# Optimization experiments

Hardware: AMD Instinct MI355X
Metric: run time of the kernel (lower is better)

## Reference

```python
import jax, jax.numpy as jnp
import numpy as np

OBS, H, F1, A, T, B = 128, 128, 256, 18, 128, 1024


def _ln(x, w, b, eps=1e-5):
    mu = jnp.mean(x, -1, keepdims=True)
    xc = x - mu
    var = jnp.mean(xc * xc, -1, keepdims=True)
    return xc * jax.lax.rsqrt(var + eps) * w + b


def _features(x, w1, b1, w2, b2, lnw, lnb):
    h = jax.nn.relu(x @ w1.T + b1)      # [N, 256]
    h = h @ w2.T + b2                   # [N, 128]
    return jax.nn.relu(_ln(h, lnw, lnb))


def _masked_lstm(xs, ds, h0, c0, wih, whh, b):
    # xs: [T,B,H], ds: [T,B] float; PyTorch gate order i,f,g,o
    def step(carry, inp):
        h, c = carry
        xt, dt = inp
        m = (1.0 - dt)[:, None]
        h = h * m
        c = c * m
        g = xt @ wih.T + h @ whh.T + b  # [B, 4H]
        i, f, gg, o = jnp.split(g, 4, axis=-1)
        c = jax.nn.sigmoid(f) * c + jax.nn.sigmoid(i) * jnp.tanh(gg)
        h = jax.nn.sigmoid(o) * jnp.tanh(c)
        return (h, c), h
    (hT, cT), hs = jax.lax.scan(step, (h0, c0), (xs, ds))
    return hs, hT, cT


def setup_inputs() -> dict:
    key = jax.random.key(0)
    ks = iter(jax.random.split(key, 64))
    p = lambda shape, s=0.05: jax.random.normal(next(ks), shape, jnp.float32) * s
    inp = {
        'x': jax.random.normal(next(ks), (T * B, OBS), jnp.float32),
        'actor_h': jnp.zeros((1, B, H), jnp.float32),
        'actor_c': jnp.zeros((1, B, H), jnp.float32),
        'critic_h': jnp.zeros((1, B, H), jnp.float32),
        'critic_c': jnp.zeros((1, B, H), jnp.float32),
        'done': jax.random.randint(next(ks), (T * B,), 0, 2, jnp.int32),
        'action': jax.random.randint(next(ks), (T * B,), 0, A, jnp.int64),
        # actor params
        'af_w1': p((F1, OBS)), 'af_b1': p((F1,)),
        'af_w2': p((H, F1)), 'af_b2': p((H,)),
        'af_lnw': jnp.ones((H,), jnp.float32), 'af_lnb': jnp.zeros((H,), jnp.float32),
        'a_wih': p((4 * H, H)), 'a_whh': p((4 * H, H)), 'a_b': p((4 * H,)),
        'a_lnw': jnp.ones((H,), jnp.float32), 'a_lnb': jnp.zeros((H,), jnp.float32),
        'a_hw': p((A, H)), 'a_hb': p((A,)),
        # critic params
        'cf_w1': p((F1, OBS)), 'cf_b1': p((F1,)),
        'cf_w2': p((H, F1)), 'cf_b2': p((H,)),
        'cf_lnw': jnp.ones((H,), jnp.float32), 'cf_lnb': jnp.zeros((H,), jnp.float32),
        'c_wih': p((4 * H, H)), 'c_whh': p((4 * H, H)), 'c_b': p((4 * H,)),
        'c_lnw': jnp.ones((H,), jnp.float32), 'c_lnb': jnp.zeros((H,), jnp.float32),
        'c_hw': p((1, H)), 'c_hb': p((1,)),
    }
    return inp


def reference(x, actor_h, actor_c, critic_h, critic_c,
              af_w1, af_b1, af_w2, af_b2, af_lnw, af_lnb,
              a_wih, a_whh, a_b, a_lnw, a_lnb, a_hw, a_hb,
              cf_w1, cf_b1, cf_w2, cf_b2, cf_lnw, cf_lnb,
              c_wih, c_whh, c_b, c_lnw, c_lnb, c_hw, c_hb,
              done, action):
    bsz = actor_h.shape[1]
    ds = done.astype(jnp.float32).reshape(-1, bsz)  # [T, B]

    # actor branch
    af = _features(x, af_w1, af_b1, af_w2, af_b2, af_lnw, af_lnb).reshape(-1, bsz, H)
    hs, ahT, acT = _masked_lstm(af, ds, actor_h[0], actor_c[0], a_wih, a_whh, a_b)
    ah = _ln(hs.reshape(-1, H), a_lnw, a_lnb)
    logits = ah @ a_hw.T + a_hb                     # [N, A]
    logp_all = jax.nn.log_softmax(logits)
    logp = jnp.take_along_axis(logp_all, action[:, None], axis=1)[:, 0]
    entropy = -jnp.sum(jnp.exp(logp_all) * logp_all, axis=-1)

    # critic branch
    cf = _features(x, cf_w1, cf_b1, cf_w2, cf_b2, cf_lnw, cf_lnb).reshape(-1, bsz, H)
    cs, chT, ccT = _masked_lstm(cf, ds, critic_h[0], critic_c[0], c_wih, c_whh, c_b)
    ch = _ln(cs.reshape(-1, H), c_lnw, c_lnb)
    value = ch @ c_hw.T + c_hb                      # [N, 1]

    return (action, logp, entropy, value,
            ahT[None], acT[None], chT[None], ccT[None])
```

## Files before the change

### kernel.cpp

```cpp
#include <hip/hip_runtime.h>
#include <stdint.h>
#include <stddef.h>

#define OBS 128
#define F1D 256
#define HD  128
#define NA  18
#define TT  128
#define BB  1024
#define NN  (TT*BB)
#define LOG2E 1.442695041f

typedef __attribute__((ext_vector_type(8))) short short8;
typedef __attribute__((ext_vector_type(4))) float f32x4;

__device__ __forceinline__ unsigned short f2bf(float f) {
  union { float f; uint32_t u; } v; v.f = f;
  uint32_t u = v.u;
  u += 0x7fffu + ((u >> 16) & 1u);
  return (unsigned short)(u >> 16);
}
__device__ __forceinline__ float bf2f(uint32_t hu) {
  union { uint32_t u; float f; } v; v.u = hu << 16;
  return v.f;
}
__device__ __forceinline__ uint32_t pk2(float lo, float hi) {
  uint32_t r;
  asm("v_cvt_pk_bf16_f32 %0, %1, %2" : "=v"(r) : "v"(lo), "v"(hi));
  return r;
}
__device__ __forceinline__ f32x4 mfma16(short8 a, short8 b, f32x4 c) {
  return __builtin_amdgcn_mfma_f32_16x16x32_bf16(a, b, c, 0, 0, 0);
}
__device__ __forceinline__ short8 cvt8(const float* p, float sc) {
  float4 a = *(const float4*)p;
  float4 b = *(const float4*)(p + 4);
  union { uint32_t u[4]; short8 s; } o;
  o.u[0] = pk2(a.x*sc, a.y*sc);
  o.u[1] = pk2(a.z*sc, a.w*sc);
  o.u[2] = pk2(b.x*sc, b.y*sc);
  o.u[3] = pk2(b.z*sc, b.w*sc);
  return o.s;
}
__device__ __forceinline__ short8 pin(short8 v) {
  int4 i = *(int4*)&v;
  asm volatile("" : "+v"(i.x), "+v"(i.y), "+v"(i.z), "+v"(i.w));
  return *(short8*)&i;
}

__global__ __launch_bounds__(512, 2) void feat_kernel(
    const float* __restrict__ x,
    const float* __restrict__ aw1, const float* __restrict__ ab1,
    const float* __restrict__ aw2, const float* __restrict__ ab2,
    const float* __restrict__ aflnw, const float* __restrict__ aflnb,
    const float* __restrict__ cw1, const float* __restrict__ cb1,
    const float* __restrict__ cw2, const float* __restrict__ cb2,
    const float* __restrict__ cflnw, const float* __restrict__ cflnb,
    unsigned short* __restrict__ featg)
{
  int g = blockIdx.x;
  int br = g >> 7;
  int chunk = g & 127;
  int base8 = chunk * 8;

  const float* w1  = br ? cw1 : aw1;
  const float* b1  = br ? cb1 : ab1;
  const float* w2  = br ? cw2 : aw2;
  const float* b2  = br ? cb2 : ab2;
  const float* flw = br ? cflnw : aflnw;
  const float* flb = br ? cflnb : aflnb;
  unsigned short* feat = featg + (size_t)br * NN * HD;

  __shared__ __align__(16) char smemA[51200];

  int tid = threadIdx.x;
  int w = tid >> 6, lane = tid & 63, q = lane >> 4, ln = lane & 15;
  int team = tid >> 8, t_tid = tid & 255, w4 = w & 3;

  unsigned short* xst  = (unsigned short*)smemA + team*4096;
  unsigned short* h1st = (unsigned short*)(smemA + 16384) + team*8192;
  float*          lnst = (float*)(smemA + 49152) + team*256;

  short8 b1f[4][4]; float b1v[4];
  #pragma unroll
  for (int ct = 0; ct < 4; ++ct) {
    int nn = w4*64 + ct*16 + ln;
    b1v[ct] = b1[nn];
    #pragma unroll
    for (int kf = 0; kf < 4; ++kf)
      b1f[ct][kf] = pin(cvt8(&w1[nn*OBS + kf*32 + q*8], 1.0f));
  }
  short8 b2f[2][8]; float b2v[2], lwv[2], lbv[2];
  #pragma unroll
  for (int nt = 0; nt < 2; ++nt) {
    int nn = w4*32 + nt*16 + ln;
    b2v[nt] = b2[nn]; lwv[nt] = flw[nn]; lbv[nt] = flb[nn];
    #pragma unroll
    for (int kf = 0; kf < 8; ++kf)
      b2f[nt][kf] = pin(cvt8(&w2[nn*F1D + kf*32 + q*8], 1.0f));
  }
  float4 xr[4];
  #pragma unroll
  for (int s = 0; s < 4; ++s) {
    int e4 = t_tid + s*256;
    int r = e4 >> 5, c4 = e4 & 31;
    size_t grow = (size_t)(team*4 + (r>>3))*BB + base8 + (r&7);
    xr[s] = ((const float4*)x)[grow*32 + c4];
  }
  for (int j = 0; j < 16; ++j) {
    int jj = j*2 + team;
    #pragma unroll
    for (int s = 0; s < 4; ++s) {
      int e = (t_tid + s*256) * 4;
      int r = e >> 7, k = e & 127;
      int ad = r*128 + ((((k>>3) ^ (r&15)) << 3)) + (k&7);
      uint2 d;
      d.x = pk2(xr[s].x, xr[s].y);
      d.y = pk2(xr[s].z, xr[s].w);
      *(uint2*)&xst[ad] = d;
    }
    __syncthreads();
    {
      int jjn = (j < 15) ? jj + 2 : jj;
      #pragma unroll
      for (int s = 0; s < 4; ++s) {
        int e4 = t_tid + s*256;
        int r = e4 >> 5, c4 = e4 & 31;
        size_t grow = (size_t)(jjn*4 + (r>>3))*BB + base8 + (r&7);
        xr[s] = ((const float4*)x)[grow*32 + c4];
      }
    }
    short8 af[2][4];
    #pragma unroll
    for (int mt = 0; mt < 2; ++mt)
      #pragma unroll
      for (int kf = 0; kf < 4; ++kf)
        af[mt][kf] = *(const short8*)&xst[(mt*16 + ln)*128 + ((((kf<<2)|q) ^ ln) << 3)];
    #pragma unroll
    for (int ct = 0; ct < 4; ++ct) {
      int nn = w4*64 + ct*16 + ln;
      #pragma unroll
      for (int mt = 0; mt < 2; ++mt) {
        f32x4 acc = {b1v[ct], b1v[ct], b1v[ct], b1v[ct]};
        #pragma unroll
        for (int kf = 0; kf < 4; ++kf) acc = mfma16(af[mt][kf], b1f[ct][kf], acc);
        float v0 = acc[0] > 0.0f ? acc[0] : 0.0f;
        float v1 = acc[1] > 0.0f ? acc[1] : 0.0f;
        float v2 = acc[2] > 0.0f ? acc[2] : 0.0f;
        float v3 = acc[3] > 0.0f ? acc[3] : 0.0f;
        uint32_t p01 = pk2(v0, v1), p23 = pk2(v2, v3);
        int r0 = mt*16 + q*4;
        h1st[(r0+0)*256 + (((nn>>3) ^ ((r0+0)&15)) << 3) + (nn&7)] = (unsigned short)p01;
        h1st[(r0+1)*256 + (((nn>>3) ^ ((r0+1)&15)) << 3) + (nn&7)] = (unsigned short)(p01 >> 16);
        h1st[(r0+2)*256 + (((nn>>3) ^ ((r0+2)&15)) << 3) + (nn&7)] = (unsigned short)p23;
        h1st[(r0+3)*256 + (((nn>>3) ^ ((r0+3)&15)) << 3) + (nn&7)] = (unsigned short)(p23 >> 16);
      }
    }
    __syncthreads();
    f32x4 acc2[2][2];
    #pragma unroll
    for (int mt = 0; mt < 2; ++mt) {
      short8 ah[8];
      #pragma unroll
      for (int kf = 0; kf < 8; ++kf)
        ah[kf] = *(const short8*)&h1st[(mt*16 + ln)*256 + ((((kf<<2)|q) ^ ln) << 3)];
      #pragma unroll
      for (int nt = 0; nt < 2; ++nt) {
        f32x4 acc = {b2v[nt], b2v[nt], b2v[nt], b2v[nt]};
        #pragma unroll
        for (int kf = 0; kf < 8; ++kf) acc = mfma16(ah[kf], b2f[nt][kf], acc);
        acc2[nt][mt] = acc;
      }
    }
    #pragma unroll
    for (int mt = 0; mt < 2; ++mt)
      #pragma unroll
      for (int rg = 0; rg < 4; ++rg) {
        float s = acc2[0][mt][rg] + acc2[1][mt][rg];
        float ssq = acc2[0][mt][rg]*acc2[0][mt][rg] + acc2[1][mt][rg]*acc2[1][mt][rg];
        #pragma unroll
        for (int m = 1; m < 16; m <<= 1) { s += __shfl_xor(s, m); ssq += __shfl_xor(ssq, m); }
        if (ln == 0) {
          int r = mt*16 + q*4 + rg;
          lnst[r*8 + w4*2]     = s;
          lnst[r*8 + w4*2 + 1] = ssq;
        }
      }
    __syncthreads();
    #pragma unroll
    for (int mt = 0; mt < 2; ++mt)
      #pragma unroll
      for (int rg = 0; rg < 4; ++rg) {
        int r = mt*16 + q*4 + rg;
        float4 p0 = *(const float4*)&lnst[r*8];
        float4 p1 = *(const float4*)&lnst[r*8 + 4];
        float S  = p0.x + p0.z + p1.x + p1.z;
        float SS = p0.y + p0.w + p1.y + p1.w;
        float mu = S * (1.0f/128.0f);
        float var = SS * (1.0f/128.0f) - mu*mu;
        float rstd = rsqrtf(var + 1e-5f);
        size_t grow = (size_t)(jj*4 + (r>>3))*BB + base8 + (r&7);
        float t0 = (acc2[0][mt][rg] - mu) * rstd * lwv[0] + lbv[0];
        float t1 = (acc2[1][mt][rg] - mu) * rstd * lwv[1] + lbv[1];
        if (t0 < 0.0f) t0 = 0.0f;
        if (t1 < 0.0f) t1 = 0.0f;
        uint32_t p = pk2(t0, t1);
        unsigned short* fp = &feat[grow*HD + w4*32 + ln];
        fp[0]  = (unsigned short)p;
        fp[16] = (unsigned short)(p >> 16);
      }
    __syncthreads();
  }
}

__global__ __launch_bounds__(512, 2) void lstm_head_kernel(
    const int* __restrict__ done, const int* __restrict__ action,
    const float* __restrict__ awih, const float* __restrict__ awhh,
    const float* __restrict__ a_b,
    const float* __restrict__ alnw, const float* __restrict__ alnb,
    const float* __restrict__ ahw, const float* __restrict__ ahb,
    const float* __restrict__ cwih, const float* __restrict__ cwhh,
    const float* __restrict__ c_b,
    const float* __restrict__ clnw, const float* __restrict__ clnb,
    const float* __restrict__ chw, const float* __restrict__ chb,
    const float* __restrict__ ah0, const float* __restrict__ ac0,
    const float* __restrict__ ch0, const float* __restrict__ cc0,
    unsigned short* __restrict__ featg, float* __restrict__ dout)
{
  int g = blockIdx.x;
  int br = g >> 7;
  int chunk = g & 127;
  int base8 = chunk * 8;

  const float* wih = br ? cwih : awih;
  const float* whh = br ? cwhh : awhh;
  const float* gb  = br ? c_b : a_b;
  const float* h0  = br ? ch0 : ah0;
  const float* c0  = br ? cc0 : ac0;
  unsigned short* feat = featg + (size_t)br * NN * HD;

  __shared__ __align__(16) char smemC[51200];
  __shared__ float mls[(TT+1)*8];
  __shared__ unsigned short hlds[2][8*128];
  __shared__ float pa[HD], pb[HD], cws[HD];
  __shared__ float hbl[NA];
  __shared__ float cbsS;
  __shared__ int flagS;

  int tid = threadIdx.x;
  int w = tid >> 6, lane = tid & 63, q = lane >> 4, ln = lane & 15;

  int n = w*16 + ln;
  {
    short8 bfr[4][8]; float bias[4];
    #pragma unroll
    for (int g4 = 0; g4 < 4; ++g4) {
      int gn = g4*128 + n;
      float sc = (g4 == 2) ? -2.0f*LOG2E : -LOG2E;
      bias[g4] = gb[gn] * sc;
      #pragma unroll
      for (int kf = 0; kf < 8; ++kf) {
        const float* src = (kf < 4) ? &wih[gn*HD + kf*32 + q*8]
                                    : &whh[gn*HD + (kf-4)*32 + q*8];
        bfr[g4][kf] = pin(cvt8(src, sc));
      }
    }
    for (int i = tid; i < (TT+1)*8; i += 512)
      mls[i] = (i < TT*8) ? 1.0f - (float)done[(i>>3)*BB + base8 + (i&7)] : 1.0f;

    const int loff = (base8 + (ln>>1))*HD + q*8;
    int soff[2], hoffw[2], haddr[4];
    #pragma unroll
    for (int j = 0; j < 2; ++j) {
      int r = q*2 + j;
      soff[j]  = (base8 + r)*HD + n;
      hoffw[j] = r*128 + (((n>>3) ^ r) << 3) + (n&7);
    }
    #pragma unroll
    for (int kf = 0; kf < 4; ++kf) {
      int rr = ln >> 1;
      haddr[kf] = rr*128 + ((((kf<<2)|q) ^ rr) << 3);
    }
    float hp[2], cp[2]; unsigned short hu_prev[2];
    #pragma unroll
    for (int j = 0; j < 2; ++j) {
      int b = base8 + q*2 + j;
      hp[j] = h0[b*HD + n];
      cp[j] = c0[b*HD + n];
      hu_prev[j] = 0;
    }
    __syncthreads();

    short8 f0[4], f1[4];
    #pragma unroll
    for (int kf = 0; kf < 4; ++kf)
      f0[kf] = *(const short8*)&feat[loff + kf*32];
    f32x4 xgA[4], xgB[4];
    #pragma unroll
    for (int g4 = 0; g4 < 4; ++g4)
      xgA[g4] = (f32x4){bias[g4], bias[g4], bias[g4], bias[g4]};
    #pragma unroll
    for (int kf = 0; kf < 4; ++kf) {
      xgA[0] = mfma16(f0[kf], bfr[0][kf], xgA[0]);
      xgA[1] = mfma16(f0[kf], bfr[1][kf], xgA[1]);
      xgA[2] = mfma16(f0[kf], bfr[2][kf], xgA[2]);
      xgA[3] = mfma16(f0[kf], bfr[3][kf], xgA[3]);
    }
    {
      const unsigned short* fq1 = feat + (size_t)1 * (BB*HD);
      #pragma unroll
      for (int kf = 0; kf < 4; ++kf)
        f1[kf] = *(const short8*)&fq1[loff + kf*32];
    }
    {
      float m0 = mls[q*2], m1 = mls[q*2 + 1];
      cp[0] *= m0; cp[1] *= m1;
      uint32_t hpk = pk2(hp[0]*m0, hp[1]*m1);
      hlds[0][hoffw[0]] = (unsigned short)hpk;
      hlds[0][hoffw[1]] = (unsigned short)(hpk >> 16);
    }
    __syncthreads();

#define LSTM_STEP(TTT, CUR, NXT, XA, XN, HB)                                   \
  {                                                                            \
    short8 hfr[4];                                                             \
    _Pragma("unroll")                                                          \
    for (int kf = 0; kf < 4; ++kf)                                             \
      hfr[kf] = *(const short8*)&hlds[HB][haddr[kf]];                          \
    if ((TTT) > 0) {                                                           \
      unsigned short* sq = feat + (size_t)((TTT) - 1) * (BB*HD);               \
      sq[soff[0]] = hu_prev[0];                                                \
      sq[soff[1]] = hu_prev[1];                                                \
    }                                                                          \
    int tn = ((TTT) + 2 < TT) ? (TTT) + 2 : TT - 1;                            \
    const unsigned short* fq = feat + (size_t)tn * (BB*HD);                    \
    _Pragma("unroll")                                                          \
    for (int kf = 0; kf < 4; ++kf)                                             \
      NXT[kf] = *(const short8*)&fq[loff + kf*32];                             \
    _Pragma("unroll")                                                          \
    for (int kf = 0; kf < 4; ++kf) {                                           \
      (XA)[0] = mfma16(hfr[kf], bfr[0][4+kf], (XA)[0]);                        \
      (XA)[1] = mfma16(hfr[kf], bfr[1][4+kf], (XA)[1]);                        \
      (XA)[2] = mfma16(hfr[kf], bfr[2][4+kf], (XA)[2]);                        \
      (XA)[3] = mfma16(hfr[kf], bfr[3][4+kf], (XA)[3]);                        \
    }                                                                          \
    (XN)[0] = (f32x4){bias[0], bias[0], bias[0], bias[0]};                     \
    (XN)[1] = (f32x4){bias[1], bias[1], bias[1], bias[1]};                     \
    (XN)[2] = (f32x4){bias[2], bias[2], bias[2], bias[2]};                     \
    (XN)[3] = (f32x4){bias[3], bias[3], bias[3], bias[3]};                     \
    _Pragma("unroll")                                                          \
    for (int kf = 0; kf < 4; ++kf) {                                           \
      (XN)[0] = mfma16(CUR[kf], bfr[0][kf], (XN)[0]);                          \
      (XN)[1] = mfma16(CUR[kf], bfr[1][kf], (XN)[1]);                          \
      (XN)[2] = mfma16(CUR[kf], bfr[2][kf], (XN)[2]);                          \
      (XN)[3] = mfma16(CUR[kf], bfr[3][kf], (XN)[3]);                          \
    }                                                                          \
    float hnv[2], cnv[2];                                                      \
    _Pragma("unroll")                                                          \
    for (int j = 0; j < 2; ++j) {                                              \
      int rg = j*2;     \
      float si = __builtin_amdgcn_rcpf(1.0f + __builtin_amdgcn_exp2f((XA)[0][rg])); \
      float sf = __builtin_amdgcn_rcpf(1.0f + __builtin_amdgcn_exp2f((XA)[1][rg])); \
      float tg = __builtin_fmaf(2.0f,                                          \
                   __builtin_amdgcn_rcpf(1.0f + __builtin_amdgcn_exp2f((XA)[2][rg])), -1.0f); \
      float so = __builtin_amdgcn_rcpf(1.0f + __builtin_amdgcn_exp2f((XA)[3][rg])); \
      float cn = __builtin_fmaf(sf, cp[j], si*tg);                             \
      float th = __builtin_fmaf(2.0f,                                          \
                   __builtin_amdgcn_rcpf(1.0f + __builtin_amdgcn_exp2f(-2.0f*LOG2E*cn)), -1.0f); \
      hnv[j] = so * th;                                                        \
      cnv[j] = cn;                                                             \
    }                                                                          \
    uint32_t hpk = pk2(hnv[0], hnv[1]);                                        \
    unsigned short hu0 = (unsigned short)hpk;                                  \
    unsigned short hu1 = (unsigned short)(hpk >> 16);                          \
    hu_prev[0] = hu0; hu_prev[1] = hu1;                                        \
    float2 mn = *(const float2*)&mls[((TTT)+1)*8 + q*2];                       \
    bool l0 = (mn.x != 0.0f), l1 = (mn.y != 0.0f);                             \
    cp[0] = l0 ? cnv[0] : 0.0f; hp[0] = hnv[0];                                \
    cp[1] = l1 ? cnv[1] : 0.0f; hp[1] = hnv[1];                                \
    hlds[(HB)^1][hoffw[0]] = l0 ? hu0 : (unsigned short)0;                     \
    hlds[(HB)^1][hoffw[1]] = l1 ? hu1 : (unsigned short)0;                     \
    __syncthreads();                                                           \
  }

    for (int t = 0; t < TT; t += 2) {
      LSTM_STEP(t,   f1, f0, xgA, xgB, 0)
      LSTM_STEP(t+1, f0, f1, xgB, xgA, 1)
    }
#undef LSTM_STEP

    {
      unsigned short* sq = feat + (size_t)(TT-1)*(BB*HD);
      sq[soff[0]] = hu_prev[0];
      sq[soff[1]] = hu_prev[1];
    }
    {
      float* outh = dout + (size_t)(4 + br*2) * NN;
      float* outc = dout + (size_t)(5 + br*2) * NN;
      #pragma unroll
      for (int j = 0; j < 2; ++j) {
        int b = base8 + q*2 + j;
        outh[b*HD + n] = hp[j];
        outc[b*HD + n] = cp[j];
      }
    }
  }

  if (tid == 0) flagS = 0;
  if (tid < HD) {
    pa[tid] = br ? clnw[tid] : alnw[tid];
    pb[tid] = br ? clnb[tid] : alnb[tid];
    if (br) cws[tid] = chw[tid];
  }
  int localf = 0;
  if (br == 0) {
    if (tid < NA) hbl[tid] = ahb[tid];
    for (int i = 2*tid + 1; i < 4096; i += 1024) localf |= action[i];
  } else if (tid == 0) cbsS = chb[0];
  __syncthreads();
  if (localf) flagS = 1;
  __syncthreads();

  int sub = tid & 3, kidx = tid >> 2;
  if (br == 0) {
    unsigned short* hsn = (unsigned short*)smemC;
    float* co = (float*)(smemC + 32768);
    short8 hbf[2][4];
    #pragma unroll
    for (int nt = 0; nt < 2; ++nt) {
      int nn = nt*16 + ln;
      #pragma unroll
      for (int kf = 0; kf < 4; ++kf) {
        short8 z = {0,0,0,0,0,0,0,0};
        hbf[nt][kf] = (nn < NA) ? pin(cvt8(&ahw[nn*HD + kf*32 + q*8], 1.0f)) : z;
      }
    }
    int fl = flagS;
    for (int ch = 0; ch < 8; ++ch) {
      {
        int k = ch*128 + kidx;
        int rrow = (k >> 3)*BB + base8 + (k & 7);
        const unsigned short* hp2 = feat + (size_t)rrow*HD + sub*32;
        uint4 d0 = *(const uint4*)hp2;
        uint4 d1 = *(const uint4*)(hp2 + 8);
        uint4 d2 = *(const uint4*)(hp2 + 16);
        uint4 d3 = *(const uint4*)(hp2 + 24);
        float nv[32];
        #define UP(W_, B_) { nv[B_] = bf2f((W_) & 0xffffu); nv[(B_)+1] = bf2f((W_) >> 16); }
        UP(d0.x,0) UP(d0.y,2) UP(d0.z,4) UP(d0.w,6)
        UP(d1.x,8) UP(d1.y,10) UP(d1.z,12) UP(d1.w,14)
        UP(d2.x,16) UP(d2.y,18) UP(d2.z,20) UP(d2.w,22)
        UP(d3.x,24) UP(d3.y,26) UP(d3.z,28) UP(d3.w,30)
        #undef UP
        float s = 0.0f, ssq = 0.0f;
        #pragma unroll
        for (int j = 0; j < 32; ++j) { s += nv[j]; ssq += nv[j]*nv[j]; }
        s += __shfl_xor(s, 1); ssq += __shfl_xor(ssq, 1);
        s += __shfl_xor(s, 2); ssq += __shfl_xor(ssq, 2);
        float mu = s * (1.0f/128.0f);
        float var = ssq * (1.0f/128.0f) - mu*mu;
        float rstd = rsqrtf(var + 1e-5f);
        #pragma unroll
        for (int cc = 0; cc < 4; ++cc) {
          float ov[8];
          #pragma unroll
          for (int j = 0; j < 8; ++j) {
            int c = sub*32 + cc*8 + j;
            ov[j] = (nv[cc*8+j] - mu) * rstd * pa[c] + pb[c];
          }
          uint4 P;
          P.x = pk2(ov[0], ov[1]); P.y = pk2(ov[2], ov[3]);
          P.z = pk2(ov[4], ov[5]); P.w = pk2(ov[6], ov[7]);
          int c8 = sub*4 + cc;
          *(uint4*)&hsn[kidx*128 + ((c8 ^ (kidx & 15)) << 3)] = P;
        }
      }
      __syncthreads();
      {
        short8 afh[4];
        #pragma unroll
        for (int kf = 0; kf < 4; ++kf)
          afh[kf] = *(const short8*)&hsn[(w*16 + ln)*128 + ((((kf<<2)|q) ^ ln) << 3)];
        #pragma unroll
        for (int nt = 0; nt < 2; ++nt) {
          f32x4 acc = {0.0f, 0.0f, 0.0f, 0.0f};
          #pragma unroll
          for (int kf = 0; kf < 4; ++kf) acc = mfma16(afh[kf], hbf[nt][kf], acc);
          #pragma unroll
          for (int rg = 0; rg < 4; ++rg)
            co[(w*16 + q*4 + rg)*36 + nt*16 + ln] = acc[rg];
        }
      }
      __syncthreads();
      if (tid < 128) {
        int k = ch*128 + tid;
        int rrow = (k >> 3)*BB + base8 + (k & 7);
        int act = fl ? action[rrow] : (int)(((const long long*)action)[rrow]);
        dout[rrow] = (float)act;
        int aidx = act < 0 ? 0 : (act > NA-1 ? NA-1 : act);
        float lg[NA];
        #pragma unroll
        for (int a = 0; a < NA; ++a) lg[a] = co[tid*36 + a] + hbl[a];
        float mx = lg[0];
        #pragma unroll
        for (int a = 1; a < NA; ++a) mx = fmaxf(mx, lg[a]);
        float se = 0.0f;
        #pragma unroll
        for (int a = 0; a < NA; ++a) se += __expf(lg[a] - mx);
        float lse = __logf(se);
        float lpa = 0.0f, ent = 0.0f;
        #pragma unroll
        for (int a = 0; a < NA; ++a) {
          float lp = lg[a] - mx - lse;
          ent -= __expf(lp) * lp;
          lpa += (a == aidx) ? lp : 0.0f;
        }
        dout[(size_t)NN + rrow] = lpa;
        dout[(size_t)2*NN + rrow] = ent;
      }
      __syncthreads();
    }
  } else {
    for (int ch = 0; ch < 8; ++ch) {
      int k = ch*128 + kidx;
      int rrow = (k >> 3)*BB + base8 + (k & 7);
      const unsigned short* hp2 = feat + (size_t)rrow*HD + sub*32;
      uint4 d0 = *(const uint4*)hp2;
      uint4 d1 = *(const uint4*)(hp2 + 8);
      uint4 d2 = *(const uint4*)(hp2 + 16);
      uint4 d3 = *(const uint4*)(hp2 + 24);
      float nv[32];
      #define UP(W_, B_) { nv[B_] = bf2f((W_) & 0xffffu); nv[(B_)+1] = bf2f((W_) >> 16); }
      UP(d0.x,0) UP(d0.y,2) UP(d0.z,4) UP(d0.w,6)
      UP(d1.x,8) UP(d1.y,10) UP(d1.z,12) UP(d1.w,14)
      UP(d2.x,16) UP(d2.y,18) UP(d2.z,20) UP(d2.w,22)
      UP(d3.x,24) UP(d3.y,26) UP(d3.z,28) UP(d3.w,30)
      #undef UP
      float s = 0.0f, ssq = 0.0f;
      #pragma unroll
      for (int j = 0; j < 32; ++j) { s += nv[j]; ssq += nv[j]*nv[j]; }
      s += __shfl_xor(s, 1); ssq += __shfl_xor(ssq, 1);
      s += __shfl_xor(s, 2); ssq += __shfl_xor(ssq, 2);
      float mu = s * (1.0f/128.0f);
      float var = ssq * (1.0f/128.0f) - mu*mu;
      float rstd = rsqrtf(var + 1e-5f);
      float dot = 0.0f;
      #pragma unroll
      for (int j = 0; j < 32; ++j) {
        int c = sub*32 + j;
        dot += ((nv[j] - mu) * rstd * pa[c] + pb[c]) * cws[c];
      }
      dot += __shfl_xor(dot, 1);
      dot += __shfl_xor(dot, 2);
      if (sub == 0) dout[(size_t)3*NN + rrow] = dot + cbsS;
    }
  }
}

extern "C" void kernel_launch(void* const* d_in, const int* in_sizes, int n_in,
                              void* d_out, int out_size, void* d_ws, size_t ws_size,
                              hipStream_t stream) {
  (void)in_sizes; (void)n_in; (void)out_size; (void)ws_size;
  const float* x    = (const float*)d_in[0];
  const float* ah0  = (const float*)d_in[1];
  const float* ac0  = (const float*)d_in[2];
  const float* ch0  = (const float*)d_in[3];
  const float* cc0  = (const float*)d_in[4];
  const int*   done = (const int*)d_in[5];
  const int*   act  = (const int*)d_in[6];
  const float* aw1  = (const float*)d_in[7];
  const float* ab1  = (const float*)d_in[8];
  const float* aw2  = (const float*)d_in[9];
  const float* ab2  = (const float*)d_in[10];
  const float* aflnw= (const float*)d_in[11];
  const float* aflnb= (const float*)d_in[12];
  const float* awih = (const float*)d_in[13];
  const float* awhh = (const float*)d_in[14];
  const float* a_b  = (const float*)d_in[15];
  const float* alnw = (const float*)d_in[16];
  const float* alnb = (const float*)d_in[17];
  const float* ahw  = (const float*)d_in[18];
  const float* ahb  = (const float*)d_in[19];
  const float* cw1  = (const float*)d_in[20];
  const float* cb1  = (const float*)d_in[21];
  const float* cw2  = (const float*)d_in[22];
  const float* cb2  = (const float*)d_in[23];
  const float* cflnw= (const float*)d_in[24];
  const float* cflnb= (const float*)d_in[25];
  const float* cwih = (const float*)d_in[26];
  const float* cwhh = (const float*)d_in[27];
  const float* c_b  = (const float*)d_in[28];
  const float* clnw = (const float*)d_in[29];
  const float* clnb = (const float*)d_in[30];
  const float* chw  = (const float*)d_in[31];
  const float* chb  = (const float*)d_in[32];

  unsigned short* featb = (unsigned short*)d_ws;
  float* out = (float*)d_out;

  feat_kernel<<<256, 512, 0, stream>>>(
      x, aw1, ab1, aw2, ab2, aflnw, aflnb,
      cw1, cb1, cw2, cb2, cflnw, cflnb, featb);

  lstm_head_kernel<<<256, 512, 0, stream>>>(
      done, act,
      awih, awhh, a_b, alnw, alnb, ahw, ahb,
      cwih, cwhh, c_b, clnw, clnb, chw, chb,
      ah0, ac0, ch0, cc0,
      featb, out);
}
```

Before: 431.7 us.

## Split LSTM and output heads into separate kernels with a wide head grid

Moves the post-LSTM layernorm, policy head, log-softmax and value head out of the 256-block recurrent kernel into a new head kernel launched with 2048 blocks, each handling 128 contiguous rows. The previous version ran the heads inside the same few blocks that ran the recurrence, serialised per block. The new layout spreads the head work across the whole GPU and frees the large head shared buffer from the LSTM kernel, which may help its occupancy. The cost is an extra launch and a re-read of the hidden states from global memory.

```diff
diff --git a/kernel.cpp b/kernel.cpp
--- a/kernel.cpp
+++ b/kernel.cpp
@@ -213,16 +213,12 @@
   }
 }
 
-__global__ __launch_bounds__(512, 2) void lstm_head_kernel(
-    const int* __restrict__ done, const int* __restrict__ action,
+__global__ __launch_bounds__(512, 2) void lstm_kernel(
+    const int* __restrict__ done,
     const float* __restrict__ awih, const float* __restrict__ awhh,
     const float* __restrict__ a_b,
-    const float* __restrict__ alnw, const float* __restrict__ alnb,
-    const float* __restrict__ ahw, const float* __restrict__ ahb,
     const float* __restrict__ cwih, const float* __restrict__ cwhh,
     const float* __restrict__ c_b,
-    const float* __restrict__ clnw, const float* __restrict__ clnb,
-    const float* __restrict__ chw, const float* __restrict__ chb,
     const float* __restrict__ ah0, const float* __restrict__ ac0,
     const float* __restrict__ ch0, const float* __restrict__ cc0,
     unsigned short* __restrict__ featg, float* __restrict__ dout)
@@ -239,87 +235,81 @@
   const float* c0  = br ? cc0 : ac0;
   unsigned short* feat = featg + (size_t)br * NN * HD;
 
-  __shared__ __align__(16) char smemC[51200];
   __shared__ float mls[(TT+1)*8];
   __shared__ unsigned short hlds[2][8*128];
-  __shared__ float pa[HD], pb[HD], cws[HD];
-  __shared__ float hbl[NA];
-  __shared__ float cbsS;
-  __shared__ int flagS;
 
   int tid = threadIdx.x;
   int w = tid >> 6, lane = tid & 63, q = lane >> 4, ln = lane & 15;
 
   int n = w*16 + ln;
+  short8 bfr[4][8]; float bias[4];
+  #pragma unroll
+  for (int g4 = 0; g4 < 4; ++g4) {
+    int gn = g4*128 + n;
+    float sc = (g4 == 2) ? -2.0f*LOG2E : -LOG2E;
+    bias[g4] = gb[gn] * sc;
+    #pragma unroll
+    for (int kf = 0; kf < 8; ++kf) {
+      const float* src = (kf < 4) ? &wih[gn*HD + kf*32 + q*8]
+                                  : &whh[gn*HD + (kf-4)*32 + q*8];
+      bfr[g4][kf] = pin(cvt8(src, sc));
+    }
+  }
+  for (int i = tid; i < (TT+1)*8; i += 512)
+    mls[i] = (i < TT*8) ? 1.0f - (float)done[(i>>3)*BB + base8 + (i&7)] : 1.0f;
+
+  const int loff = (base8 + (ln>>1))*HD + q*8;
+  int soff[2], hoffw[2], haddr[4];
+  #pragma unroll
+  for (int j = 0; j < 2; ++j) {
+    int r = q*2 + j;
+    soff[j]  = (base8 + r)*HD + n;
+    hoffw[j] = r*128 + (((n>>3) ^ r) << 3) + (n&7);
+  }
+  #pragma unroll
+  for (int kf = 0; kf < 4; ++kf) {
+    int rr = ln >> 1;
+    haddr[kf] = rr*128 + ((((kf<<2)|q) ^ rr) << 3);
+  }
+  float hp[2], cp[2]; unsigned short hu_prev[2];
+  #pragma unroll
+  for (int j = 0; j < 2; ++j) {
+    int b = base8 + q*2 + j;
+    hp[j] = h0[b*HD + n];
+    cp[j] = c0[b*HD + n];
+    hu_prev[j] = 0;
+  }
+  __syncthreads();
+
+  short8 f0[4], f1[4];
+  #pragma unroll
+  for (int kf = 0; kf < 4; ++kf)
+    f0[kf] = *(const short8*)&feat[loff + kf*32];
+  f32x4 xgA[4], xgB[4];
+  #pragma unroll
+  for (int g4 = 0; g4 < 4; ++g4)
+    xgA[g4] = (f32x4){bias[g4], bias[g4], bias[g4], bias[g4]};
+  #pragma unroll
+  for (int kf = 0; kf < 4; ++kf) {
+    xgA[0] = mfma16(f0[kf], bfr[0][kf], xgA[0]);
+    xgA[1] = mfma16(f0[kf], bfr[1][kf], xgA[1]);
+    xgA[2] = mfma16(f0[kf], bfr[2][kf], xgA[2]);
+    xgA[3] = mfma16(f0[kf], bfr[3][kf], xgA[3]);
+  }
   {
-    short8 bfr[4][8]; float bias[4];
-    #pragma unroll
-    for (int g4 = 0; g4 < 4; ++g4) {
-      int gn = g4*128 + n;
-      float sc = (g4 == 2) ? -2.0f*LOG2E : -LOG2E;
-      bias[g4] = gb[gn] * sc;
-      #pragma unroll
-      for (int kf = 0; kf < 8; ++kf) {
-        const float* src = (kf < 4) ? &wih[gn*HD + kf*32 + q*8]
-                                    : &whh[gn*HD + (kf-4)*32 + q*8];
-        bfr[g4][kf] = pin(cvt8(src, sc));
-      }
-    }
-    for (int i = tid; i < (TT+1)*8; i += 512)
-      mls[i] = (i < TT*8) ? 1.0f - (float)done[(i>>3)*BB + base8 + (i&7)] : 1.0f;
-
-    const int loff = (base8 + (ln>>1))*HD + q*8;
-    int soff[2], hoffw[2], haddr[4];
-    #pragma unroll
-    for (int j = 0; j < 2; ++j) {
-      int r = q*2 + j;
-      soff[j]  = (base8 + r)*HD + n;
-      hoffw[j] = r*128 + (((n>>3) ^ r) << 3) + (n&7);
-    }
-    #pragma unroll
-    for (int kf = 0; kf < 4; ++kf) {
-      int rr = ln >> 1;
-      haddr[kf] = rr*128 + ((((kf<<2)|q) ^ rr) << 3);
-    }
-    float hp[2], cp[2]; unsigned short hu_prev[2];
-    #pragma unroll
-    for (int j = 0; j < 2; ++j) {
-      int b = base8 + q*2 + j;
-      hp[j] = h0[b*HD + n];
-      cp[j] = c0[b*HD + n];
-      hu_prev[j] = 0;
-    }
-    __syncthreads();
-
-    short8 f0[4], f1[4];
+    const unsigned short* fq1 = feat + (size_t)1 * (BB*HD);
     #pragma unroll
     for (int kf = 0; kf < 4; ++kf)
-      f0[kf] = *(const short8*)&feat[loff + kf*32];
-    f32x4 xgA[4], xgB[4];
-    #pragma unroll
-    for (int g4 = 0; g4 < 4; ++g4)
-      xgA[g4] = (f32x4){bias[g4], bias[g4], bias[g4], bias[g4]};
-    #pragma unroll
-    for (int kf = 0; kf < 4; ++kf) {
-      xgA[0] = mfma16(f0[kf], bfr[0][kf], xgA[0]);
-      xgA[1] = mfma16(f0[kf], bfr[1][kf], xgA[1]);
-      xgA[2] = mfma16(f0[kf], bfr[2][kf], xgA[2]);
-      xgA[3] = mfma16(f0[kf], bfr[3][kf], xgA[3]);
-    }
-    {
-      const unsigned short* fq1 = feat + (size_t)1 * (BB*HD);
-      #pragma unroll
-      for (int kf = 0; kf < 4; ++kf)
-        f1[kf] = *(const short8*)&fq1[loff + kf*32];
-    }
-    {
-      float m0 = mls[q*2], m1 = mls[q*2 + 1];
-      cp[0] *= m0; cp[1] *= m1;
-      uint32_t hpk = pk2(hp[0]*m0, hp[1]*m1);
-      hlds[0][hoffw[0]] = (unsigned short)hpk;
-      hlds[0][hoffw[1]] = (unsigned short)(hpk >> 16);
-    }
-    __syncthreads();
+      f1[kf] = *(const short8*)&fq1[loff + kf*32];
+  }
+  {
+    float m0 = mls[q*2], m1 = mls[q*2 + 1];
+    cp[0] *= m0; cp[1] *= m1;
+    uint32_t hpk = pk2(hp[0]*m0, hp[1]*m1);
+    hlds[0][hoffw[0]] = (unsigned short)hpk;
+    hlds[0][hoffw[1]] = (unsigned short)(hpk >> 16);
+  }
+  __syncthreads();
 
 #define LSTM_STEP(TTT, CUR, NXT, XA, XN, HB)                                   \
   {                                                                            \
@@ -383,28 +373,51 @@
     __syncthreads();                                                           \
   }
 
-    for (int t = 0; t < TT; t += 2) {
-      LSTM_STEP(t,   f1, f0, xgA, xgB, 0)
-      LSTM_STEP(t+1, f0, f1, xgB, xgA, 1)
-    }
+  for (int t = 0; t < TT; t += 2) {
+    LSTM_STEP(t,   f1, f0, xgA, xgB, 0)
+    LSTM_STEP(t+1, f0, f1, xgB, xgA, 1)
+  }
 #undef LSTM_STEP
 
-    {
-      unsigned short* sq = feat + (size_t)(TT-1)*(BB*HD);
-      sq[soff[0]] = hu_prev[0];
-      sq[soff[1]] = hu_prev[1];
-    }
-    {
-      float* outh = dout + (size_t)(4 + br*2) * NN;
-      float* outc = dout + (size_t)(5 + br*2) * NN;
-      #pragma unroll
-      for (int j = 0; j < 2; ++j) {
-        int b = base8 + q*2 + j;
-        outh[b*HD + n] = hp[j];
-        outc[b*HD + n] = cp[j];
-      }
-    }
-  }
+  {
+    unsigned short* sq = feat + (size_t)(TT-1)*(BB*HD);
+    sq[soff[0]] = hu_prev[0];
+    sq[soff[1]] = hu_prev[1];
+  }
+  {
+    float* outh = dout + (size_t)(4 + br*2) * NN;
+    float* outc = dout + (size_t)(5 + br*2) * NN;
+    #pragma unroll
+    for (int j = 0; j < 2; ++j) {
+      int b = base8 + q*2 + j;
+      outh[b*HD + n] = hp[j];
+      outc[b*HD + n] = cp[j];
+    }
+  }
+}
+
+__global__ __launch_bounds__(512, 2) void head_kernel(
+    const int* __restrict__ action,
+    const float* __restrict__ alnw, const float* __restrict__ alnb,
+    const float* __restrict__ ahw, const float* __restrict__ ahb,
+    const float* __restrict__ clnw, const float* __restrict__ clnb,
+    const float* __restrict__ chw, const float* __restrict__ chb,
+    const unsigned short* __restrict__ featg, float* __restrict__ dout)
+{
+  int g = blockIdx.x;
+  int br = g >> 10;
+  int r0 = (g & 1023) * 128;
+  const unsigned short* feat = featg + (size_t)br * NN * HD;
+
+  __shared__ __align__(16) char smemC[51200];
+  __shared__ float pa[HD], pb[HD], cws[HD];
+  __shared__ float hbl[NA];
+  __shared__ float cbsS;
+  __shared__ int flagS;
+
+  int tid = threadIdx.x;
+  int w = tid >> 6, lane = tid & 63, q = lane >> 4, ln = lane & 15;
+  int sub = tid & 3, kidx = tid >> 2;
 
   if (tid == 0) flagS = 0;
   if (tid < HD) {
@@ -421,7 +434,6 @@
   if (localf) flagS = 1;
   __syncthreads();
 
-  int sub = tid & 3, kidx = tid >> 2;
   if (br == 0) {
     unsigned short* hsn = (unsigned short*)smemC;
     float* co = (float*)(smemC + 32768);
@@ -436,95 +448,9 @@
       }
     }
     int fl = flagS;
-    for (int ch = 0; ch < 8; ++ch) {
-      {
-        int k = ch*128 + kidx;
-        int rrow = (k >> 3)*BB + base8 + (k & 7);
-        const unsigned short* hp2 = feat + (size_t)rrow*HD + sub*32;
-        uint4 d0 = *(const uint4*)hp2;
-        uint4 d1 = *(const uint4*)(hp2 + 8);
-        uint4 d2 = *(const uint4*)(hp2 + 16);
-        uint4 d3 = *(const uint4*)(hp2 + 24);
-        float nv[32];
-        #define UP(W_, B_) { nv[B_] = bf2f((W_) & 0xffffu); nv[(B_)+1] = bf2f((W_) >> 16); }
-        UP(d0.x,0) UP(d0.y,2) UP(d0.z,4) UP(d0.w,6)
-        UP(d1.x,8) UP(d1.y,10) UP(d1.z,12) UP(d1.w,14)
-        UP(d2.x,16) UP(d2.y,18) UP(d2.z,20) UP(d2.w,22)
-        UP(d3.x,24) UP(d3.y,26) UP(d3.z,28) UP(d3.w,30)
-        #undef UP
-        float s = 0.0f, ssq = 0.0f;
-        #pragma unroll
-        for (int j = 0; j < 32; ++j) { s += nv[j]; ssq += nv[j]*nv[j]; }
-        s += __shfl_xor(s, 1); ssq += __shfl_xor(ssq, 1);
-        s += __shfl_xor(s, 2); ssq += __shfl_xor(ssq, 2);
-        float mu = s * (1.0f/128.0f);
-        float var = ssq * (1.0f/128.0f) - mu*mu;
-        float rstd = rsqrtf(var + 1e-5f);
-        #pragma unroll
-        for (int cc = 0; cc < 4; ++cc) {
-          float ov[8];
-          #pragma unroll
-          for (int j = 0; j < 8; ++j) {
-            int c = sub*32 + cc*8 + j;
-            ov[j] = (nv[cc*8+j] - mu) * rstd * pa[c] + pb[c];
-          }
-          uint4 P;
-          P.x = pk2(ov[0], ov[1]); P.y = pk2(ov[2], ov[3]);
-          P.z = pk2(ov[4], ov[5]); P.w = pk2(ov[6], ov[7]);
-          int c8 = sub*4 + cc;
-          *(uint4*)&hsn[kidx*128 + ((c8 ^ (kidx & 15)) << 3)] = P;
-        }
-      }
-      __syncthreads();
-      {
-        short8 afh[4];
-        #pragma unroll
-        for (int kf = 0; kf < 4; ++kf)
-          afh[kf] = *(const short8*)&hsn[(w*16 + ln)*128 + ((((kf<<2)|q) ^ ln) << 3)];
-        #pragma unroll
-        for (int nt = 0; nt < 2; ++nt) {
-          f32x4 acc = {0.0f, 0.0f, 0.0f, 0.0f};
-          #pragma unroll
-          for (int kf = 0; kf < 4; ++kf) acc = mfma16(afh[kf], hbf[nt][kf], acc);
-          #pragma unroll
-          for (int rg = 0; rg < 4; ++rg)
-            co[(w*16 + q*4 + rg)*36 + nt*16 + ln] = acc[rg];
-        }
-      }
-      __syncthreads();
-      if (tid < 128) {
-        int k = ch*128 + tid;
-        int rrow = (k >> 3)*BB + base8 + (k & 7);
-        int act = fl ? action[rrow] : (int)(((const long long*)action)[rrow]);
-        dout[rrow] = (float)act;
-        int aidx = act < 0 ? 0 : (act > NA-1 ? NA-1 : act);
-        float lg[NA];
-        #pragma unroll
-        for (int a = 0; a < NA; ++a) lg[a] = co[tid*36 + a] + hbl[a];
-        float mx = lg[0];
-        #pragma unroll
-        for (int a = 1; a < NA; ++a) mx = fmaxf(mx, lg[a]);
-        float se = 0.0f;
-        #pragma unroll
-        for (int a = 0; a < NA; ++a) se += __expf(lg[a] - mx);
-        float lse = __logf(se);
-        float lpa = 0.0f, ent = 0.0f;
-        #pragma unroll
-        for (int a = 0; a < NA; ++a) {
-          float lp = lg[a] - mx - lse;
-          ent -= __expf(lp) * lp;
-          lpa += (a == aidx) ? lp : 0.0f;
-        }
-        dout[(size_t)NN + rrow] = lpa;
-        dout[(size_t)2*NN + rrow] = ent;
-      }
-      __syncthreads();
-    }
-  } else {
-    for (int ch = 0; ch < 8; ++ch) {
-      int k = ch*128 + kidx;
-      int rrow = (k >> 3)*BB + base8 + (k & 7);
-      const unsigned short* hp2 = feat + (size_t)rrow*HD + sub*32;
+    {
+      int r = r0 + kidx;
+      const unsigned short* hp2 = feat + (size_t)r*HD + sub*32;
       uint4 d0 = *(const uint4*)hp2;
       uint4 d1 = *(const uint4*)(hp2 + 8);
       uint4 d2 = *(const uint4*)(hp2 + 16);
@@ -544,16 +470,94 @@
       float mu = s * (1.0f/128.0f);
       float var = ssq * (1.0f/128.0f) - mu*mu;
       float rstd = rsqrtf(var + 1e-5f);
-      float dot = 0.0f;
-      #pragma unroll
-      for (int j = 0; j < 32; ++j) {
-        int c = sub*32 + j;
-        dot += ((nv[j] - mu) * rstd * pa[c] + pb[c]) * cws[c];
-      }
-      dot += __shfl_xor(dot, 1);
-      dot += __shfl_xor(dot, 2);
-      if (sub == 0) dout[(size_t)3*NN + rrow] = dot + cbsS;
-    }
+      #pragma unroll
+      for (int cc = 0; cc < 4; ++cc) {
+        float ov[8];
+        #pragma unroll
+        for (int j = 0; j < 8; ++j) {
+          int c = sub*32 + cc*8 + j;
+          ov[j] = (nv[cc*8+j] - mu) * rstd * pa[c] + pb[c];
+        }
+        uint4 P;
+        P.x = pk2(ov[0], ov[1]); P.y = pk2(ov[2], ov[3]);
+        P.z = pk2(ov[4], ov[5]); P.w = pk2(ov[6], ov[7]);
+        int c8 = sub*4 + cc;
+        *(uint4*)&hsn[kidx*128 + ((c8 ^ (kidx & 15)) << 3)] = P;
+      }
+    }
+    __syncthreads();
+    {
+      short8 afh[4];
+      #pragma unroll
+      for (int kf = 0; kf < 4; ++kf)
+        afh[kf] = *(const short8*)&hsn[(w*16 + ln)*128 + ((((kf<<2)|q) ^ ln) << 3)];
+      #pragma unroll
+      for (int nt = 0; nt < 2; ++nt) {
+        f32x4 acc = {0.0f, 0.0f, 0.0f, 0.0f};
+        #pragma unroll
+        for (int kf = 0; kf < 4; ++kf) acc = mfma16(afh[kf], hbf[nt][kf], acc);
+        #pragma unroll
+        for (int rg = 0; rg < 4; ++rg)
+          co[(w*16 + q*4 + rg)*36 + nt*16 + ln] = acc[rg];
+      }
+    }
+    __syncthreads();
+    if (tid < 128) {
+      int r = r0 + tid;
+      int act = fl ? action[r] : (int)(((const long long*)action)[r]);
+      dout[r] = (float)act;
+      int aidx = act < 0 ? 0 : (act > NA-1 ? NA-1 : act);
+      float lg[NA];
+      #pragma unroll
+      for (int a = 0; a < NA; ++a) lg[a] = co[tid*36 + a] + hbl[a];
+      float mx = lg[0];
+      #pragma unroll
+      for (int a = 1; a < NA; ++a) mx = fmaxf(mx, lg[a]);
+      float se = 0.0f;
+      #pragma unroll
+      for (int a = 0; a < NA; ++a) se += __expf(lg[a] - mx);
+      float lse = __logf(se);
+      float lpa = 0.0f, ent = 0.0f;
+      #pragma unroll
+      for (int a = 0; a < NA; ++a) {
+        float lp = lg[a] - mx - lse;
+        ent -= __expf(lp) * lp;
+        lpa += (a == aidx) ? lp : 0.0f;
+      }
+      dout[(size_t)NN + r] = lpa;
+      dout[(size_t)2*NN + r] = ent;
+    }
+  } else {
+    int r = r0 + kidx;
+    const unsigned short* hp2 = feat + (size_t)r*HD + sub*32;
+    uint4 d0 = *(const uint4*)hp2;
+    uint4 d1 = *(const uint4*)(hp2 + 8);
+    uint4 d2 = *(const uint4*)(hp2 + 16);
+    uint4 d3 = *(const uint4*)(hp2 + 24);
+    float nv[32];
+    #define UP(W_, B_) { nv[B_] = bf2f((W_) & 0xffffu); nv[(B_)+1] = bf2f((W_) >> 16); }
+    UP(d0.x,0) UP(d0.y,2) UP(d0.z,4) UP(d0.w,6)
+    UP(d1.x,8) UP(d1.y,10) UP(d1.z,12) UP(d1.w,14)
+    UP(d2.x,16) UP(d2.y,18) UP(d2.z,20) UP(d2.w,22)
+    UP(d3.x,24) UP(d3.y,26) UP(d3.z,28) UP(d3.w,30)
+    #undef UP
+    float s = 0.0f, ssq = 0.0f;
+    #pragma unroll
+    for (int j = 0; j < 32; ++j) { s += nv[j]; ssq += nv[j]*nv[j]; }
+    s += __shfl_xor(s, 1); ssq += __shfl_xor(ssq, 1);
+    s += __shfl_xor(s, 2); ssq += __shfl_xor(ssq, 2);
+    float mu = s * (1.0f/128.0f);
+    float var = ssq * (1.0f/128.0f) - mu*mu;
+    float rstd = rsqrtf(var + 1e-5f);
+    float dot = 0.0f;
+    #pragma unroll
+    for (int j = 0; j < 32; ++j) {
+      int c = sub*32 + j;
+      dot += ((nv[j] - mu) * rstd * pa[c] + pb[c]) * cws[c];
+    }
+    dot += __shfl_xor(dot, 1);
+    dot += __shfl_xor(dot, 2);
+    if (sub == 0) dout[(size_t)3*NN + r] = dot + cbsS;
   }
 }
 
@@ -602,10 +606,15 @@
       x, aw1, ab1, aw2, ab2, aflnw, aflnb,
       cw1, cb1, cw2, cb2, cflnw, cflnb, featb);
 
-  lstm_head_kernel<<<256, 512, 0, stream>>>(
-      done, act,
-      awih, awhh, a_b, alnw, alnb, ahw, ahb,
-      cwih, cwhh, c_b, clnw, clnb, chw, chb,
+  lstm_kernel<<<256, 512, 0, stream>>>(
+      done,
+      awih, awhh, a_b, cwih, cwhh, c_b,
       ah0, ac0, ch0, cc0,
       featb, out);
-}
+
+  head_kernel<<<2048, 512, 0, stream>>>(
+      act,
+      alnw, alnb, ahw, ahb,
+      clnw, clnb, chw, chb,
+      featb, out);
+}
```

Result: no change. 437.2 us (+1.3%).
